# Kernel optimization log

Measured on AMD Instinct MI355X. Metric: run time of the kernel, lower is better.

The kernel has to match this reference:

```python
import jax, jax.numpy as jnp
import numpy as np

B, S, D = 4, 4096, 2048      # batch, seq, model_dim
E = 128                      # emb_dim (hardcoded in module)
H = 128                      # head_dim
TAU = 0.4                    # self.T
BASE = 3.0                   # self.base (gumbel-sigmoid offset)
LN_EPS = 1e-5


def setup_inputs() -> dict:
    key = jax.random.key(0)
    k_x, k_wr, k_wd, k_g = jax.random.split(key, 4)
    x = jax.random.normal(k_x, (B, S, D), dtype=jnp.float32)
    # torch nn.Linear stores weight as [out_features, in_features]
    W_router = jax.random.normal(k_wr, (E, D), dtype=jnp.float32) / np.sqrt(D)
    W_decoder = jax.random.normal(k_wd, (H, E), dtype=jnp.float32) / np.sqrt(E)
    ln_gamma = jnp.ones((E,), dtype=jnp.float32)
    ln_beta = jnp.zeros((E,), dtype=jnp.float32)
    rnn_state = jnp.zeros((E,), dtype=jnp.float32)  # registered buffer, zeros
    # torch: gumbels = -Exp(1).log()  -> standard Gumbel(0,1) noise
    u = jax.random.uniform(k_g, (B, S, H), dtype=jnp.float32, minval=1e-20, maxval=1.0)
    gumbel_noise = -jnp.log(-jnp.log(u))
    return {
        "x": x, "W_router": W_router, "W_decoder": W_decoder,
        "ln_gamma": ln_gamma, "ln_beta": ln_beta, "rnn_state": rnn_state,
        "gumbel_noise": gumbel_noise, "top_k": 32,
    }


def reference(x, W_router, W_decoder, ln_gamma, ln_beta, rnn_state, gumbel_noise, top_k):
    # router linear (no bias): [B,S,D] @ [D,E] -> [B,S,E]
    out = jnp.einsum("bsd,ed->bse", x, W_router)
    full_emb = rnn_state + out
    # LayerNorm over emb dim (biased variance, as torch LayerNorm)
    mu = full_emb.mean(-1, keepdims=True)
    var = full_emb.var(-1, keepdims=True)
    h = (full_emb - mu) / jnp.sqrt(var + LN_EPS) * ln_gamma + ln_beta
    # decoder linear after exact GELU: [B,S,E] @ [E,H] -> [B,S,H]
    logits = jnp.einsum("bse,he->bsh", jax.nn.gelu(h, approximate=False), W_decoder)
    # gumbel-sigmoid (soft): sigmoid((logits + gumbel + offset)/tau)
    binary_approx = jax.nn.sigmoid((logits + gumbel_noise + BASE) / TAU)
    # hard_sample: straight-through round
    binary = jax.lax.stop_gradient(jnp.round(binary_approx) - binary_approx) + binary_approx
    # top-k mask over head_dim
    _, topk_idx = jax.lax.top_k(binary_approx, top_k)            # [B,S,top_k]
    topk_mask = jax.nn.one_hot(topk_idx, H, dtype=binary_approx.dtype).sum(-2)  # [B,S,H]
    cnt = binary.sum(-1, keepdims=True)
    binary = jnp.where(cnt > top_k, topk_mask, binary)
    # fallback: if a token selects nothing, pick argmax of soft scores
    zero_mask = binary.sum(-1, keepdims=True) == 0
    fallback = jax.nn.one_hot(jnp.argmax(binary_approx, axis=-1), H, dtype=binary_approx.dtype)
    binary = jnp.where(zero_mask, fallback, binary)
    binary = binary.reshape(B, S, -1, H)  # [B,S,1,H]
    return binary, binary_approx
```

## Files before the change

kernel.cpp:

```cpp
#include <hip/hip_runtime.h>
#include <math.h>

#define NTOK   16384
#define DDIM   2048
#define EDIM   128
#define HDIM   128
#define TOKT   64
#define NRND   16
#define KRND   128

typedef __attribute__((ext_vector_type(8)))  _Float16 half8;
typedef __attribute__((ext_vector_type(16))) float    f32x16;

#define MFMA32 __builtin_amdgcn_mfma_f32_32x32x16_f16

__device__ __forceinline__ int swz(int t, int e) {
  return t * EDIM + ((e & 96) | ((e ^ t) & 31));
}

__device__ __forceinline__ void cvt8(const float4& a, const float4& b,
                                     half8& h, half8& l) {
#pragma unroll
  for (int m = 0; m < 4; ++m) {
    const float v = (&a.x)[m];
    const _Float16 hv = (_Float16)v;
    h[m] = hv; l[m] = (_Float16)((v - (float)hv) * 2048.0f);
  }
#pragma unroll
  for (int m = 0; m < 4; ++m) {
    const float v = (&b.x)[m];
    const _Float16 hv = (_Float16)v;
    h[m + 4] = hv; l[m + 4] = (_Float16)((v - (float)hv) * 2048.0f);
  }
}

__global__ __launch_bounds__(256)
void conv_w(const float* __restrict__ Wr,
            _Float16* __restrict__ wh, _Float16* __restrict__ wl) {
  const int idx  = (int)blockIdx.x * 256 + (int)threadIdx.x;
  const int lane = idx & 63;
  const int ks   = (idx >> 6) & 127;
  const int nt   = idx >> 13;
  const int n    = nt * 32 + (lane & 31);
  const int k0   = ks * 16 + (lane >> 5) * 8;
  half8 h, l;
#pragma unroll
  for (int j = 0; j < 8; ++j) {
    const float w = Wr[(size_t)n * DDIM + k0 + j] * 32.0f;
    const _Float16 hh = (_Float16)w;
    h[j] = hh;
    l[j] = (_Float16)((w - (float)hh) * 2048.0f);
  }
  *(half8*)(wh + (size_t)idx * 8) = h;
  *(half8*)(wl + (size_t)idx * 8) = l;
}

__global__ __launch_bounds__(1024, 4)
void fused_router(const float* __restrict__ x,
                  const _Float16* __restrict__ wsh,
                  const _Float16* __restrict__ wsl,
                  const float* __restrict__ Wd,
                  const float* __restrict__ gamma,
                  const float* __restrict__ beta,
                  const float* __restrict__ rnn,
                  const float* __restrict__ gum,
                  float* __restrict__ outb,
                  float* __restrict__ outa) {
  __shared__ char smraw[65536];
  char* const sm = smraw;
  float* const A  = (float*)smraw;
  float* const G4 = (float*)(smraw + 32768);

  const int tid  = (int)threadIdx.x;
  const int wv   = __builtin_amdgcn_readfirstlane(tid >> 6);
  const int lane = tid & 63;
  const int t0   = (int)blockIdx.x * TOKT;

  const int kw  = wv >> 3;
  const int mt  = (wv >> 2) & 1;
  const int nt  = wv & 3;
  const int kw4 = kw * 4;

  const int s_tok = (tid & 3) + ((tid >> 6) << 2);
  const int s_kq  = (tid >> 2) & 15;
  const int s_s   = s_kq >> 1;
  const int s_ko  = s_kq & 1;
  const float* xg = x + (size_t)(t0 + s_tok) * DDIM + s_kq * 8;
  const int wbase = (s_s * 2 + (s_tok >> 5)) * 2048;
  const int wslot = ((s_ko * 32 + (s_tok & 31)) ^ s_s ^ (s_ko * 4)) * 16;

  const size_t wbf = (size_t)nt * 65536 + (size_t)lane * 8;

  f32x16 hh, cr;
#pragma unroll
  for (int g = 0; g < 16; ++g) { hh[g] = 0.0f; cr[g] = 0.0f; }

  {
    const float4 a0 = *(const float4*)(xg + 0);
    const float4 a1 = *(const float4*)(xg + 4);
    half8 h, l;
    cvt8(a0, a1, h, l);
    *(half8*)(sm + wbase + wslot)        = h;
    *(half8*)(sm + wbase + 1024 + wslot) = l;
  }

  for (int r = 0; r < NRND; ++r) {
    __syncthreads();
    float4 p0, p1;
    if (r + 1 < NRND) {
      const float* xn = xg + (r + 1) * KRND;
      p0 = *(const float4*)(xn + 0);
      p1 = *(const float4*)(xn + 4);
    }
    const char* bb = sm + (r & 1) * 32768;
#pragma unroll
    for (int i = 0; i < 4; ++i) {
      const int s  = kw4 + i;
      const int fb = (s * 2 + mt) * 2048;
      const int ai = ((lane ^ s ^ ((lane >> 5) << 2)) << 4);
      const half8 ah = *(const half8*)(bb + fb + ai);
      const half8 al = *(const half8*)(bb + fb + 1024 + ai);
      const size_t wo = wbf + (size_t)(r * 8 + s) * 512;
      const half8 bh = *(const half8*)(wsh + wo);
      const half8 bl = *(const half8*)(wsl + wo);
      hh = MFMA32(ah, bh, hh, 0, 0, 0);
      cr = MFMA32(ah, bl, cr, 0, 0, 0);
      cr = MFMA32(al, bh, cr, 0, 0, 0);
    }
    if (r + 1 < NRND) {
      half8 h, l;
      cvt8(p0, p1, h, l);
      char* dst = sm + ((r + 1) & 1) * 32768;
      *(half8*)(dst + wbase + wslot)        = h;
      *(half8*)(dst + wbase + 1024 + wslot) = l;
    }
  }
  __syncthreads();

  const int e = nt * 32 + (lane & 31);
  if (kw == 0) {
#pragma unroll
    for (int g = 0; g < 16; ++g) {
      const int row = (g & 3) + 8 * (g >> 2) + 4 * (lane >> 5);
      A[swz(mt * 32 + row, e)] =
          hh[g] * (1.0f / 32.0f) + cr[g] * (1.0f / 65536.0f);
    }
  }
  __syncthreads();
  if (kw == 1) {
    const float rv = rnn[e];
#pragma unroll
    for (int g = 0; g < 16; ++g) {
      const int row = (g & 3) + 8 * (g >> 2) + 4 * (lane >> 5);
      A[swz(mt * 32 + row, e)] +=
          hh[g] * (1.0f / 32.0f) + cr[g] * (1.0f / 65536.0f) + rv;
    }
  }
  __syncthreads();

  const int e0 = wv * 8;
  {
    const float gm0 = gamma[lane], gm1 = gamma[lane + 64];
    const float bt0 = beta[lane],  bt1 = beta[lane + 64];
    for (int tt = wv * 4; tt < wv * 4 + 4; ++tt) {
      const float v0 = A[swz(tt, lane)];
      const float v1 = A[swz(tt, lane + 64)];
      float s = v0 + v1;
#pragma unroll
      for (int m = 32; m; m >>= 1) s += __shfl_xor(s, m);
      const float mu = s * (1.0f / 128.0f);
      const float d0 = v0 - mu, d1 = v1 - mu;
      float q = d0 * d0 + d1 * d1;
#pragma unroll
      for (int m = 32; m; m >>= 1) q += __shfl_xor(q, m);
      const float rstd = 1.0f / sqrtf(q * (1.0f / 128.0f) + 1e-5f);
      const float h0v = d0 * rstd * gm0 + bt0;
      const float h1v = d1 * rstd * gm1 + bt1;
      const float g0 = 0.5f * h0v * (1.0f + erff(h0v * 0.70710678118654752f));
      const float g1 = 0.5f * h1v * (1.0f + erff(h1v * 0.70710678118654752f));
      const int e0a = lane, e1a = lane + 64;
      G4[(tt * 32 + (((e0a >> 2) ^ (tt & 31)))) * 4 + (e0a & 3)] = g0;
      G4[(tt * 32 + (((e1a >> 2) ^ (tt & 31)))) * 4 + (e1a & 3)] = g1;
    }
  }
  __syncthreads();

  {
    float acc2[8];
#pragma unroll
    for (int j = 0; j < 8; ++j) acc2[j] = 0.0f;
    const float4* wd4 = (const float4*)(Wd + (size_t)e0 * EDIM);
#pragma unroll 2
    for (int kg = 0; kg < EDIM / 4; ++kg) {
      const float4 gv = *(const float4*)&G4[(lane * 32 + (kg ^ (lane & 31))) * 4];
#pragma unroll
      for (int j = 0; j < 8; ++j) {
        const float4 w = wd4[(size_t)j * (EDIM / 4) + kg];
        acc2[j] = fmaf(gv.x, w.x,
                  fmaf(gv.y, w.y,
                  fmaf(gv.z, w.z,
                  fmaf(gv.w, w.w, acc2[j]))));
      }
    }
    __syncthreads();
#pragma unroll
    for (int j = 0; j < 8; ++j) A[swz(lane, e0 + j)] = acc2[j];
  }
  __syncthreads();

  for (int tt = wv * 4; tt < wv * 4 + 4; ++tt) {
    const size_t T = (size_t)(t0 + tt);
    const float l0 = A[swz(tt, lane)];
    const float l1 = A[swz(tt, lane + 64)];
    const float gn0 = gum[T * HDIM + lane];
    const float gn1 = gum[T * HDIM + lane + 64];
    const float z0 = (l0 + gn0 + 3.0f) * 2.5f;
    const float z1 = (l1 + gn1 + 3.0f) * 2.5f;
    const float ba0 = 1.0f / (1.0f + expf(-z0));
    const float ba1 = 1.0f / (1.0f + expf(-z1));
    const unsigned ub0 = __float_as_uint(ba0);
    const unsigned ub1 = __float_as_uint(ba1);
    const int r0 = ba0 > 0.5f;
    const int r1 = ba1 > 0.5f;
    const int cnt = __popcll(__ballot(r0)) + __popcll(__ballot(r1));
    float bin0, bin1;
    if (cnt > 32) {
      unsigned v = 0x3F000000u;
#pragma unroll
      for (int b = 23; b >= 0; --b) {
        const unsigned cand = v | (1u << b);
        const int cc = __popcll(__ballot(ub0 >= cand)) + __popcll(__ballot(ub1 >= cand));
        if (cc >= 32) v = cand;
      }
      const int cgt = __popcll(__ballot(ub0 > v)) + __popcll(__ballot(ub1 > v));
      const int r = 32 - cgt;
      const unsigned long long t0b = __ballot(ub0 == v);
      const unsigned long long t1b = __ballot(ub1 == v);
      const int n0 = __popcll(t0b);
      const unsigned long long mlt = (1ull << lane) - 1ull;
      const int rk0 = __popcll(t0b & mlt);
      const int rk1 = n0 + __popcll(t1b & mlt);
      bin0 = (ub0 > v || (ub0 == v && rk0 < r)) ? 1.0f : 0.0f;
      bin1 = (ub1 > v || (ub1 == v && rk1 < r)) ? 1.0f : 0.0f;
    } else if (cnt == 0) {
      float m = fmaxf(ba0, ba1);
#pragma unroll
      for (int mm = 32; mm; mm >>= 1) m = fmaxf(m, __shfl_xor(m, mm));
      const unsigned long long e0b = __ballot(ba0 == m);
      const unsigned long long e1b = __ballot(ba1 == m);
      const int hstar = e0b ? (__ffsll((unsigned long long)e0b) - 1)
                            : (64 + __ffsll((unsigned long long)e1b) - 1);
      bin0 = (lane == hstar) ? 1.0f : 0.0f;
      bin1 = (lane + 64 == hstar) ? 1.0f : 0.0f;
    } else {
      bin0 = r0 ? 1.0f : 0.0f;
      bin1 = r1 ? 1.0f : 0.0f;
    }
    outb[T * HDIM + lane]      = bin0;
    outb[T * HDIM + lane + 64] = bin1;
    outa[T * HDIM + lane]      = ba0;
    outa[T * HDIM + lane + 64] = ba1;
  }
}

extern "C" void kernel_launch(void* const* d_in, const int* in_sizes, int n_in,
                              void* d_out, int out_size, void* d_ws, size_t ws_size,
                              hipStream_t stream) {
  (void)in_sizes; (void)n_in; (void)ws_size; (void)out_size;
  const float* x   = (const float*)d_in[0];
  const float* Wr  = (const float*)d_in[1];
  const float* Wd  = (const float*)d_in[2];
  const float* gm  = (const float*)d_in[3];
  const float* bt  = (const float*)d_in[4];
  const float* rnn = (const float*)d_in[5];
  const float* gum = (const float*)d_in[6];
  float* outb = (float*)d_out;
  float* outa = outb + (size_t)NTOK * HDIM;

  _Float16* wh = (_Float16*)d_ws;
  _Float16* wl = wh + (size_t)EDIM * DDIM;

  conv_w<<<dim3(128), dim3(256), 0, stream>>>(Wr, wh, wl);
  fused_router<<<dim3(NTOK / TOKT), dim3(1024), 0, stream>>>(
      x, wh, wl, Wd, gm, bt, rnn, gum, outb, outa);
}
```

Measured before the change: 256.1 us.

## Halve token tile to 32 and split K four ways across waves

Each block now handles 32 tokens instead of 64, which doubles the number of blocks. The 16 waves are regrouped into 4 K-split groups by 4 N-tiles, each group doing 2 k-steps per round, and the four partial sums are reduced through shared memory. Only half the threads stage x into smaller double buffers, and the LayerNorm and decoder phases are re-partitioned to match. The launch-bounds hint moves from 4 to 8. The aim is more parallelism and better latency hiding across CUs. The costs are an extra cross-wave reduction, re-reading the decoder weights for twice as many blocks, and idle staging threads.

```diff
diff --git a/kernel.cpp b/kernel.cpp
--- a/kernel.cpp
+++ b/kernel.cpp
@@ -5,7 +5,7 @@
 #define DDIM   2048
 #define EDIM   128
 #define HDIM   128
-#define TOKT   64
+#define TOKT   32
 #define NRND   16
 #define KRND   128
 
@@ -55,7 +55,7 @@
   *(half8*)(wl + (size_t)idx * 8) = l;
 }
 
-__global__ __launch_bounds__(1024, 4)
+__global__ __launch_bounds__(1024, 8)
 void fused_router(const float* __restrict__ x,
                   const _Float16* __restrict__ wsh,
                   const _Float16* __restrict__ wsl,
@@ -69,25 +69,27 @@
   __shared__ char smraw[65536];
   char* const sm = smraw;
   float* const A  = (float*)smraw;
-  float* const G4 = (float*)(smraw + 32768);
+  float* const S1 = (float*)(smraw + 16384);
+  float* const S2 = (float*)(smraw + 32768);
+  float* const S3 = (float*)(smraw + 49152);
+  float* const G4 = (float*)(smraw + 16384);
 
   const int tid  = (int)threadIdx.x;
   const int wv   = __builtin_amdgcn_readfirstlane(tid >> 6);
   const int lane = tid & 63;
   const int t0   = (int)blockIdx.x * TOKT;
 
-  const int kw  = wv >> 3;
-  const int mt  = (wv >> 2) & 1;
-  const int nt  = wv & 3;
-  const int kw4 = kw * 4;
-
-  const int s_tok = (tid & 3) + ((tid >> 6) << 2);
-  const int s_kq  = (tid >> 2) & 15;
-  const int s_s   = s_kq >> 1;
-  const int s_ko  = s_kq & 1;
-  const float* xg = x + (size_t)(t0 + s_tok) * DDIM + s_kq * 8;
-  const int wbase = (s_s * 2 + (s_tok >> 5)) * 2048;
-  const int wslot = ((s_ko * 32 + (s_tok & 31)) ^ s_s ^ (s_ko * 4)) * 16;
+  const int kw = wv >> 2;
+  const int nt = wv & 3;
+
+  const bool stg   = tid < 512;
+  const int  s_tok = (tid & 3) + ((tid >> 6) << 2);
+  const int  s_kq  = (tid >> 2) & 15;
+  const int  s_s   = s_kq >> 1;
+  const int  s_ko  = s_kq & 1;
+  const float* xg  = x + (size_t)(t0 + s_tok) * DDIM + s_kq * 8;
+  const int  wbase = s_s * 2048;
+  const int  wslot = ((s_ko * 32 + s_tok) ^ s_s ^ (s_ko * 4)) * 16;
 
   const size_t wbf = (size_t)nt * 65536 + (size_t)lane * 8;
 
@@ -95,7 +97,7 @@
 #pragma unroll
   for (int g = 0; g < 16; ++g) { hh[g] = 0.0f; cr[g] = 0.0f; }
 
-  {
+  if (stg) {
     const float4 a0 = *(const float4*)(xg + 0);
     const float4 a1 = *(const float4*)(xg + 4);
     half8 h, l;
@@ -107,16 +109,16 @@
   for (int r = 0; r < NRND; ++r) {
     __syncthreads();
     float4 p0, p1;
-    if (r + 1 < NRND) {
+    if (stg && r + 1 < NRND) {
       const float* xn = xg + (r + 1) * KRND;
       p0 = *(const float4*)(xn + 0);
       p1 = *(const float4*)(xn + 4);
     }
-    const char* bb = sm + (r & 1) * 32768;
-#pragma unroll
-    for (int i = 0; i < 4; ++i) {
-      const int s  = kw4 + i;
-      const int fb = (s * 2 + mt) * 2048;
+    const char* bb = sm + (r & 1) * 16384;
+#pragma unroll
+    for (int i = 0; i < 2; ++i) {
+      const int s  = kw * 2 + i;
+      const int fb = s * 2048;
       const int ai = ((lane ^ s ^ ((lane >> 5) << 2)) << 4);
       const half8 ah = *(const half8*)(bb + fb + ai);
       const half8 al = *(const half8*)(bb + fb + 1024 + ai);
@@ -127,42 +129,51 @@
       cr = MFMA32(ah, bl, cr, 0, 0, 0);
       cr = MFMA32(al, bh, cr, 0, 0, 0);
     }
-    if (r + 1 < NRND) {
+    if (stg && r + 1 < NRND) {
       half8 h, l;
       cvt8(p0, p1, h, l);
-      char* dst = sm + ((r + 1) & 1) * 32768;
+      char* dst = sm + ((r + 1) & 1) * 16384;
       *(half8*)(dst + wbase + wslot)        = h;
       *(half8*)(dst + wbase + 1024 + wslot) = l;
     }
   }
   __syncthreads();
 
-  const int e = nt * 32 + (lane & 31);
-  if (kw == 0) {
-#pragma unroll
-    for (int g = 0; g < 16; ++g) {
-      const int row = (g & 3) + 8 * (g >> 2) + 4 * (lane >> 5);
-      A[swz(mt * 32 + row, e)] =
-          hh[g] * (1.0f / 32.0f) + cr[g] * (1.0f / 65536.0f);
-    }
-  }
-  __syncthreads();
-  if (kw == 1) {
-    const float rv = rnn[e];
-#pragma unroll
-    for (int g = 0; g < 16; ++g) {
-      const int row = (g & 3) + 8 * (g >> 2) + 4 * (lane >> 5);
-      A[swz(mt * 32 + row, e)] +=
-          hh[g] * (1.0f / 32.0f) + cr[g] * (1.0f / 65536.0f) + rv;
-    }
-  }
-  __syncthreads();
-
-  const int e0 = wv * 8;
+  {
+    const int e = nt * 32 + (lane & 31);
+    float v[16];
+#pragma unroll
+    for (int g = 0; g < 16; ++g)
+      v[g] = hh[g] * (1.0f / 32.0f) + cr[g] * (1.0f / 65536.0f);
+    if (kw == 1) {
+#pragma unroll
+      for (int g = 0; g < 16; ++g)
+        S1[swz((g & 3) + 8 * (g >> 2) + 4 * (lane >> 5), e)] = v[g];
+    } else if (kw == 2) {
+#pragma unroll
+      for (int g = 0; g < 16; ++g)
+        S2[swz((g & 3) + 8 * (g >> 2) + 4 * (lane >> 5), e)] = v[g];
+    } else if (kw == 3) {
+#pragma unroll
+      for (int g = 0; g < 16; ++g)
+        S3[swz((g & 3) + 8 * (g >> 2) + 4 * (lane >> 5), e)] = v[g];
+    }
+    __syncthreads();
+    if (kw == 0) {
+      const float rv = rnn[e];
+#pragma unroll
+      for (int g = 0; g < 16; ++g) {
+        const int idx = swz((g & 3) + 8 * (g >> 2) + 4 * (lane >> 5), e);
+        A[idx] = v[g] + S1[idx] + S2[idx] + S3[idx] + rv;
+      }
+    }
+  }
+  __syncthreads();
+
   {
     const float gm0 = gamma[lane], gm1 = gamma[lane + 64];
     const float bt0 = beta[lane],  bt1 = beta[lane + 64];
-    for (int tt = wv * 4; tt < wv * 4 + 4; ++tt) {
+    for (int tt = wv * 2; tt < wv * 2 + 2; ++tt) {
       const float v0 = A[swz(tt, lane)];
       const float v1 = A[swz(tt, lane + 64)];
       float s = v0 + v1;
@@ -179,22 +190,22 @@
       const float g0 = 0.5f * h0v * (1.0f + erff(h0v * 0.70710678118654752f));
       const float g1 = 0.5f * h1v * (1.0f + erff(h1v * 0.70710678118654752f));
       const int e0a = lane, e1a = lane + 64;
-      G4[(tt * 32 + (((e0a >> 2) ^ (tt & 31)))) * 4 + (e0a & 3)] = g0;
-      G4[(tt * 32 + (((e1a >> 2) ^ (tt & 31)))) * 4 + (e1a & 3)] = g1;
+      G4[(tt * 32 + (((e0a >> 2) ^ tt))) * 4 + (e0a & 3)] = g0;
+      G4[(tt * 32 + (((e1a >> 2) ^ tt))) * 4 + (e1a & 3)] = g1;
     }
   }
   __syncthreads();
 
   {
-    float acc2[8];
-#pragma unroll
-    for (int j = 0; j < 8; ++j) acc2[j] = 0.0f;
-    const float4* wd4 = (const float4*)(Wd + (size_t)e0 * EDIM);
+    float acc2[4] = {0.0f, 0.0f, 0.0f, 0.0f};
+    const int tokn  = lane & 31;
+    const int rbase = wv * 8 + (lane >> 5) * 4;
+    const float4* wd4 = (const float4*)(Wd + (size_t)rbase * EDIM);
 #pragma unroll 2
     for (int kg = 0; kg < EDIM / 4; ++kg) {
-      const float4 gv = *(const float4*)&G4[(lane * 32 + (kg ^ (lane & 31))) * 4];
-#pragma unroll
-      for (int j = 0; j < 8; ++j) {
+      const float4 gv = *(const float4*)&G4[(tokn * 32 + (kg ^ tokn)) * 4];
+#pragma unroll
+      for (int j = 0; j < 4; ++j) {
         const float4 w = wd4[(size_t)j * (EDIM / 4) + kg];
         acc2[j] = fmaf(gv.x, w.x,
                   fmaf(gv.y, w.y,
@@ -204,11 +215,11 @@
     }
     __syncthreads();
 #pragma unroll
-    for (int j = 0; j < 8; ++j) A[swz(lane, e0 + j)] = acc2[j];
-  }
-  __syncthreads();
-
-  for (int tt = wv * 4; tt < wv * 4 + 4; ++tt) {
+    for (int j = 0; j < 4; ++j) A[swz(tokn, rbase + j)] = acc2[j];
+  }
+  __syncthreads();
+
+  for (int tt = wv * 2; tt < wv * 2 + 2; ++tt) {
     const size_t T = (size_t)(t0 + tt);
     const float l0 = A[swz(tt, lane)];
     const float l1 = A[swz(tt, lane + 64)];
```

After: 264.4 us. 1.03x slower.

## Warp-specialize router GEMM into producer and consumer waves with 4-stage LDS ring

Applied to the files above, without the earlier changes.

Splits the block into 8 producer waves and 8 MFMA consumer waves. Producers load x, convert it to hi/lo fp16 and write a 4-deep LDS ring buffer. The two sides synchronize through LDS counters polled with s_sleep instead of block-wide barriers. Consumer waves now cover the whole K range per round, which removes the split-K reduction through LDS. This aims to overlap global loads with MFMA work and cut barrier stalls, but LDS use grows to about 128KB, which likely limits residency to one block per CU, and the spin-waits add latency.

```diff
diff --git a/kernel.cpp b/kernel.cpp
--- a/kernel.cpp
+++ b/kernel.cpp
@@ -66,95 +66,114 @@
                   const float* __restrict__ gum,
                   float* __restrict__ outb,
                   float* __restrict__ outa) {
-  __shared__ char smraw[65536];
+  __shared__ char smraw[131200];
   char* const sm = smraw;
   float* const A  = (float*)smraw;
   float* const G4 = (float*)(smraw + 32768);
+  int* const prod_cnt = (int*)(smraw + 131072);
+  int* const cons_cnt = prod_cnt + 16;
 
   const int tid  = (int)threadIdx.x;
   const int wv   = __builtin_amdgcn_readfirstlane(tid >> 6);
   const int lane = tid & 63;
   const int t0   = (int)blockIdx.x * TOKT;
 
-  const int kw  = wv >> 3;
-  const int mt  = (wv >> 2) & 1;
-  const int nt  = wv & 3;
-  const int kw4 = kw * 4;
-
-  const int s_tok = (tid & 3) + ((tid >> 6) << 2);
-  const int s_kq  = (tid >> 2) & 15;
-  const int s_s   = s_kq >> 1;
-  const int s_ko  = s_kq & 1;
-  const float* xg = x + (size_t)(t0 + s_tok) * DDIM + s_kq * 8;
-  const int wbase = (s_s * 2 + (s_tok >> 5)) * 2048;
-  const int wslot = ((s_ko * 32 + (s_tok & 31)) ^ s_s ^ (s_ko * 4)) * 16;
-
-  const size_t wbf = (size_t)nt * 65536 + (size_t)lane * 8;
-
-  f32x16 hh, cr;
-#pragma unroll
-  for (int g = 0; g < 16; ++g) { hh[g] = 0.0f; cr[g] = 0.0f; }
-
-  {
-    const float4 a0 = *(const float4*)(xg + 0);
-    const float4 a1 = *(const float4*)(xg + 4);
-    half8 h, l;
-    cvt8(a0, a1, h, l);
-    *(half8*)(sm + wbase + wslot)        = h;
-    *(half8*)(sm + wbase + 1024 + wslot) = l;
-  }
-
-  for (int r = 0; r < NRND; ++r) {
+  if (tid < 32) prod_cnt[tid] = 0;
+  __syncthreads();
+
+  if (wv < 8) {
+    const int mw = wv >> 2;
+    const int nt = wv & 3;
+    const size_t wbf = (size_t)nt * 65536 + (size_t)lane * 8;
+
+    f32x16 hh, cr;
+#pragma unroll
+    for (int g = 0; g < 16; ++g) { hh[g] = 0.0f; cr[g] = 0.0f; }
+
+    for (int r = 0; r < NRND; ++r) {
+      {
+        volatile int* pf = &prod_cnt[r];
+        while (*pf < 4) __builtin_amdgcn_s_sleep(1);
+      }
+      asm volatile("" ::: "memory");
+      __builtin_amdgcn_sched_barrier(0);
+      const char* bb = sm + (r & 3) * 32768;
+#pragma unroll
+      for (int s = 0; s < 8; ++s) {
+        const int fb = (s * 2 + mw) * 2048;
+        const int ai = ((lane ^ s ^ ((lane >> 5) << 2)) << 4);
+        const half8 ah = *(const half8*)(bb + fb + ai);
+        const half8 al = *(const half8*)(bb + fb + 1024 + ai);
+        const size_t wo = wbf + (size_t)(r * 8 + s) * 512;
+        const half8 bh = *(const half8*)(wsh + wo);
+        const half8 bl = *(const half8*)(wsl + wo);
+        hh = MFMA32(ah, bh, hh, 0, 0, 0);
+        cr = MFMA32(ah, bl, cr, 0, 0, 0);
+        cr = MFMA32(al, bh, cr, 0, 0, 0);
+      }
+      __threadfence_block();
+      if (lane == 0) atomicAdd(&cons_cnt[r], 1);
+    }
     __syncthreads();
-    float4 p0, p1;
-    if (r + 1 < NRND) {
-      const float* xn = xg + (r + 1) * KRND;
-      p0 = *(const float4*)(xn + 0);
-      p1 = *(const float4*)(xn + 4);
-    }
-    const char* bb = sm + (r & 1) * 32768;
-#pragma unroll
-    for (int i = 0; i < 4; ++i) {
-      const int s  = kw4 + i;
-      const int fb = (s * 2 + mt) * 2048;
-      const int ai = ((lane ^ s ^ ((lane >> 5) << 2)) << 4);
-      const half8 ah = *(const half8*)(bb + fb + ai);
-      const half8 al = *(const half8*)(bb + fb + 1024 + ai);
-      const size_t wo = wbf + (size_t)(r * 8 + s) * 512;
-      const half8 bh = *(const half8*)(wsh + wo);
-      const half8 bl = *(const half8*)(wsl + wo);
-      hh = MFMA32(ah, bh, hh, 0, 0, 0);
-      cr = MFMA32(ah, bl, cr, 0, 0, 0);
-      cr = MFMA32(al, bh, cr, 0, 0, 0);
-    }
-    if (r + 1 < NRND) {
-      half8 h, l;
-      cvt8(p0, p1, h, l);
-      char* dst = sm + ((r + 1) & 1) * 32768;
-      *(half8*)(dst + wbase + wslot)        = h;
-      *(half8*)(dst + wbase + 1024 + wslot) = l;
-    }
-  }
-  __syncthreads();
-
-  const int e = nt * 32 + (lane & 31);
-  if (kw == 0) {
-#pragma unroll
-    for (int g = 0; g < 16; ++g) {
-      const int row = (g & 3) + 8 * (g >> 2) + 4 * (lane >> 5);
-      A[swz(mt * 32 + row, e)] =
-          hh[g] * (1.0f / 32.0f) + cr[g] * (1.0f / 65536.0f);
-    }
-  }
-  __syncthreads();
-  if (kw == 1) {
-    const float rv = rnn[e];
-#pragma unroll
-    for (int g = 0; g < 16; ++g) {
-      const int row = (g & 3) + 8 * (g >> 2) + 4 * (lane >> 5);
-      A[swz(mt * 32 + row, e)] +=
-          hh[g] * (1.0f / 32.0f) + cr[g] * (1.0f / 65536.0f) + rv;
-    }
+
+    {
+      const int e = nt * 32 + (lane & 31);
+      const float rv = rnn[e];
+#pragma unroll
+      for (int g = 0; g < 16; ++g) {
+        const int row = (g & 3) + 8 * (g >> 2) + 4 * (lane >> 5);
+        A[swz(mw * 32 + row, e)] =
+            hh[g] * (1.0f / 32.0f) + cr[g] * (1.0f / 65536.0f) + rv;
+      }
+    }
+  } else {
+    const int pw = wv - 8;
+    const int g  = pw >> 2;
+    const int gt = (pw & 3) * 64 + lane;
+    const int t  = gt >> 2;
+    const int kb = gt & 3;
+    const float* xg = x + (size_t)(t0 + t) * DDIM + kb * 32;
+    const int mtb  = (t >> 5);
+
+    float4 qa[8], qb[8];
+    auto pload = [&](int rr, float4* q) {
+#pragma unroll
+      for (int p = 0; p < 8; ++p)
+        q[p] = *(const float4*)(xg + (size_t)rr * KRND + p * 4);
+    };
+    auto pwrite = [&](int rr, const float4* q) {
+      if (rr >= 4) {
+        volatile int* cf = &cons_cnt[rr - 4];
+        while (*cf < 8) __builtin_amdgcn_s_sleep(1);
+      }
+      asm volatile("" ::: "memory");
+      __builtin_amdgcn_sched_barrier(0);
+      char* sb = sm + (rr & 3) * 32768;
+#pragma unroll
+      for (int p = 0; p < 4; ++p) {
+        const int s  = kb * 2 + (p >> 1);
+        const int ko = p & 1;
+        half8 h, l;
+        cvt8(q[2 * p], q[2 * p + 1], h, l);
+        const int base = (s * 2 + mtb) * 2048;
+        const int slot = ((ko * 32 + (t & 31)) ^ s ^ (ko * 4)) * 16;
+        *(half8*)(sb + base + slot)        = h;
+        *(half8*)(sb + base + 1024 + slot) = l;
+      }
+      __threadfence_block();
+      if (lane == 0) atomicAdd(&prod_cnt[rr], 1);
+    };
+
+    pload(g, qa);
+    pload(g + 2, qb);
+#pragma unroll
+    for (int i = 0; i < 8; i += 2) {
+      pwrite(g + 2 * i, qa);
+      if (i + 2 < 8) pload(g + 2 * (i + 2), qa);
+      pwrite(g + 2 * (i + 1), qb);
+      if (i + 3 < 8) pload(g + 2 * (i + 3), qb);
+    }
+    __syncthreads();
   }
   __syncthreads();
 
```

Result: faster. 249.3 us (-2.6%).
